# Kernel optimization log

Measured on AMD Instinct MI355X. Metric: run time of the kernel, lower is better.

Reference implementation:

```python
import jax, jax.numpy as jnp
import numpy as np

NUM_DEPTH_CANDIDATES = 32
CLAMP_MIN_DEPTH = 1e-3


def _vb(x):
    # rearrange 'b v ... -> (v b) ...'
    return jnp.reshape(jnp.swapaxes(x, 0, 1), (x.shape[0] * x.shape[1],) + x.shape[2:])


def _grid_sample_bilinear(img, u, v):
    # img: (N, C, H, W); u, v: (N, M) normalized to [-1, 1]; align_corners=True, zero padding
    N, C, H, W = img.shape
    ix = (u + 1.0) * 0.5 * (W - 1)
    iy = (v + 1.0) * 0.5 * (H - 1)
    x0 = jnp.floor(ix); y0 = jnp.floor(iy)
    x1 = x0 + 1.0; y1 = y0 + 1.0
    wx1 = ix - x0; wx0 = 1.0 - wx1
    wy1 = iy - y0; wy0 = 1.0 - wy1
    imgf = img.reshape(N, C, H * W)

    def gather(xi, yi):
        valid = (xi >= 0) & (xi <= W - 1) & (yi >= 0) & (yi <= H - 1)
        xc = jnp.clip(xi, 0, W - 1).astype(jnp.int32)
        yc = jnp.clip(yi, 0, H - 1).astype(jnp.int32)
        lin = yc * W + xc  # (N, M)
        vals = jax.vmap(lambda im, i: jnp.take(im, i, axis=1))(imgf, lin)  # (N, C, M)
        return vals * valid[:, None, :].astype(img.dtype)

    out = (gather(x0, y0) * (wx0 * wy0)[:, None, :]
           + gather(x1, y0) * (wx1 * wy0)[:, None, :]
           + gather(x0, y1) * (wx0 * wy1)[:, None, :]
           + gather(x1, y1) * (wx1 * wy1)[:, None, :])
    return out  # (N, C, M)


def _warp_with_pose_depth(feat1, pose, depth):
    # feat1: (N, C, H, W); pose: (N, 4, 4); depth: (N, D, H, W)
    N, C, H, W = feat1.shape
    D = depth.shape[1]
    two_pi = 2.0 * jnp.pi
    theta = (jnp.arange(W, dtype=jnp.float32) + 0.5) * (two_pi / W)  # longitude (W,)
    phi = (jnp.arange(H, dtype=jnp.float32) + 0.5) * (jnp.pi / H)    # colatitude (H,)
    sphi = jnp.sin(phi)[:, None]
    dirs = jnp.stack([sphi * jnp.sin(theta)[None, :],
                      jnp.broadcast_to(jnp.cos(phi)[:, None], (H, W)),
                      sphi * jnp.cos(theta)[None, :]], axis=-1)  # (H, W, 3) unit rays
    pts = depth[..., None] * dirs[None, None]                    # (N, D, H, W, 3)
    R = pose[:, :3, :3]
    t = pose[:, :3, 3]
    ptsw = jnp.einsum('nij,ndhwj->ndhwi', R, pts) + t[:, None, None, None, :]
    r = jnp.maximum(jnp.linalg.norm(ptsw, axis=-1), CLAMP_MIN_DEPTH)
    phi_w = jnp.arccos(jnp.clip(ptsw[..., 1] / r, -1.0, 1.0))
    theta_w = jnp.mod(jnp.arctan2(ptsw[..., 0], ptsw[..., 2]), two_pi)
    # spherical_2_equi then pixel->normalized [-1,1]
    u = theta_w / two_pi * 2.0 - 1.0
    v = phi_w / jnp.pi * 2.0 - 1.0
    M = D * H * W
    sampled = _grid_sample_bilinear(feat1, u.reshape(N, M), v.reshape(N, M))
    return sampled.reshape(N, C, D, H, W)


def _forward(features, extrinsics, near, far):
    b, v, c, h, w = features.shape  # v == 2
    feat0 = _vb(features)                       # (vb, c, h, w) reference features
    feat1 = _vb(features[:, ::-1])              # (vb, c, h, w) other-view features
    E0 = extrinsics[:, 0]
    E1 = extrinsics[:, 1]
    pose = jnp.linalg.inv(E1) @ E0              # ref->tgt (b,4,4)
    poses = jnp.concatenate([pose, jnp.linalg.inv(pose)], axis=0)  # (vb,4,4)
    # inverse-depth candidates, rearrange 'b v -> (v b) 1'
    mind = 1.0 / jnp.reshape(far.T, (-1, 1))
    maxd = 1.0 / jnp.reshape(near.T, (-1, 1))
    lin = jnp.linspace(0.0, 1.0, NUM_DEPTH_CANDIDATES, dtype=jnp.float32)
    depth_candi = 1.0 / (mind + lin[None, :] * (maxd - mind))  # (vb, D)
    depth = jnp.broadcast_to(depth_candi[:, :, None, None], (v * b, NUM_DEPTH_CANDIDATES, h, w))
    warped = _warp_with_pose_depth(feat1, poses, depth)        # (vb, c, D, h, w)
    corr = jnp.einsum('nchw,ncdhw->ndhw', feat0, warped) / (c ** 0.5)
    return corr  # (vb, D, h, w) plane-sweep cost volume


def setup_inputs() -> dict:
    key = jax.random.key(0)
    k1, k2, k3 = jax.random.split(key, 3)
    B, V, C, H, W = 1, 2, 128, 64, 128
    features = jax.random.normal(k1, (B, V, C, H, W), dtype=jnp.float32)
    # proper SE(3) extrinsics: random rotation via QR + small translation
    m = jax.random.normal(k2, (B, V, 3, 3), dtype=jnp.float32)
    q, _ = jnp.linalg.qr(m)
    q = q * jnp.linalg.det(q)[..., None, None]  # det +1
    t = jax.random.normal(k3, (B, V, 3), dtype=jnp.float32) * 0.1
    E = (jnp.zeros((B, V, 4, 4), dtype=jnp.float32)
         .at[..., :3, :3].set(q)
         .at[..., :3, 3].set(t)
         .at[..., 3, 3].set(1.0))
    near = jnp.full((B, V), 0.5, dtype=jnp.float32)
    far = jnp.full((B, V), 10.0, dtype=jnp.float32)
    return {"features": features, "extrinsics": E, "near": near, "far": far}


def reference(features, extrinsics, near, far):
    return _forward(features, extrinsics, near, far)
```

## Files before the change

### kernel.cpp

```cpp
#include <hip/hip_runtime.h>
#include <math.h>

#define V_ 2
#define C_ 128
#define H_ 64
#define W_ 128
#define D_ 32
#define HW_ (H_*W_)
#define PIXELS (V_*HW_)

#define PI_F 3.14159265358979323846f
#define TWO_PI_F 6.28318530717958647692f


__global__ __launch_bounds__(256) void transpose_kernel(const float* __restrict__ f,
                                                        float* __restrict__ T) {
  __shared__ float tile[64][W_ + 2];
  const int b = blockIdx.x;
  const int chalf = b & 1;
  const int h = (b >> 1) & (H_ - 1);
  const int v = b >> 7;
  const int c0 = chalf * 64;
  const int t = threadIdx.x;

  const float* src = f + (((size_t)(v * C_ + c0)) * H_ + h) * W_;
  {
    const int w2 = t & 63;
    const int cb = t >> 6;
#pragma unroll
    for (int p = 0; p < 16; ++p) {
      const int c = cb + p * 4;
      const float2 x = *(const float2*)(src + (size_t)c * HW_ + w2 * 2);
      tile[c][w2 * 2]     = x.x;
      tile[c][w2 * 2 + 1] = x.y;
    }
  }
  __syncthreads();
  float* dst = T + (((size_t)v * H_ + h) * W_) * C_ + c0;
  {
    const int c2 = t & 31;
    const int w0 = t >> 5;
#pragma unroll
    for (int p = 0; p < 16; ++p) {
      const int w = w0 + p * 8;
      float2 o;
      o.x = tile[2 * c2][w];
      o.y = tile[2 * c2 + 1][w];
      *(float2*)(dst + (size_t)w * C_ + 2 * c2) = o;
    }
  }
}

__device__ __forceinline__ float bperm_f(int byte_idx, float x) {
  return __int_as_float(__builtin_amdgcn_ds_bpermute(byte_idx, __float_as_int(x)));
}

__global__ __launch_bounds__(256, 4) void corr_kernel(const float* __restrict__ T,
                                                      const float* __restrict__ ex,
                                                      const float* __restrict__ nearp,
                                                      const float* __restrict__ farp,
                                                      float* __restrict__ out) {
  const int lane = threadIdx.x & 63;
  const int pix  = blockIdx.x * 4 + (threadIdx.x >> 6);
  const int n   = pix >> 13;
  const int rem = pix & 8191;
  const int h   = rem >> 7;
  const int w   = rem & 127;
  const int cg  = lane >> 5;
  const int cl  = lane & 31;

  const float* F0 = T + (size_t)n       * HW_ * C_;
  const float* F1 = T + (size_t)(1 - n) * HW_ * C_;

  const float4 f0v = *(const float4*)(F0 + ((size_t)(h * W_ + w)) * C_ + cl * 4);

  float PR[9], PT[3];
  {
    float R0[9], R1[9];
#pragma unroll
    for (int r = 0; r < 3; ++r)
#pragma unroll
      for (int c = 0; c < 3; ++c) {
        R0[r * 3 + c] = ex[r * 4 + c];
        R1[r * 3 + c] = ex[16 + r * 4 + c];
      }
    const float d0 = ex[3]  - ex[19];
    const float d1 = ex[7]  - ex[23];
    const float d2 = ex[11] - ex[27];
#pragma unroll
    for (int i = 0; i < 3; ++i) {
#pragma unroll
      for (int c = 0; c < 3; ++c)
        PR[i * 3 + c] = R1[i] * R0[c] + R1[3 + i] * R0[3 + c] + R1[6 + i] * R0[6 + c];
      PT[i] = R1[i] * d0 + R1[3 + i] * d1 + R1[6 + i] * d2;
    }
  }
  float Rm[9], tv[3];
  if (n == 0) {
#pragma unroll
    for (int i = 0; i < 9; ++i) Rm[i] = PR[i];
#pragma unroll
    for (int i = 0; i < 3; ++i) tv[i] = PT[i];
  } else {
#pragma unroll
    for (int r = 0; r < 3; ++r)
#pragma unroll
      for (int c = 0; c < 3; ++c) Rm[r * 3 + c] = PR[c * 3 + r];
#pragma unroll
    for (int r = 0; r < 3; ++r)
      tv[r] = -(PR[r] * PT[0] + PR[3 + r] * PT[1] + PR[6 + r] * PT[2]);
  }

  const float theta = ((float)w + 0.5f) * (TWO_PI_F / (float)W_);
  const float phi   = ((float)h + 0.5f) * (PI_F / (float)H_);
  const float sphi = sinf(phi);
  const float dx_ = sphi * sinf(theta);
  const float dy_ = cosf(phi);
  const float dz_ = sphi * cosf(theta);
  const float rdx = Rm[0] * dx_ + Rm[1] * dy_ + Rm[2] * dz_;
  const float rdy = Rm[3] * dx_ + Rm[4] * dy_ + Rm[5] * dz_;
  const float rdz = Rm[6] * dx_ + Rm[7] * dy_ + Rm[8] * dz_;

  const float mind = 1.f / farp[n];
  const float maxd = 1.f / nearp[n];
  const float depth = 1.f / (mind + ((float)cl / 31.f) * (maxd - mind));
  const float px = depth * rdx + tv[0];
  const float py = depth * rdy + tv[1];
  const float pz = depth * rdz + tv[2];
  float r = sqrtf(px * px + py * py + pz * pz);
  r = fmaxf(r, 0.001f);
  const float cy = fminf(fmaxf(py / r, -1.f), 1.f);
  const float phiw = acosf(cy);
  float thw = atan2f(px, pz);
  if (thw < 0.f) thw += TWO_PI_F;
  const float ix = thw * ((float)(W_ - 1) / TWO_PI_F);
  const float iy = phiw * ((float)(H_ - 1) / PI_F);

  const float x0f = floorf(ix), y0f = floorf(iy);
  const float x1f = x0f + 1.f,  y1f = y0f + 1.f;
  const float wx1 = ix - x0f, wx0 = 1.f - wx1;
  const float wy1 = iy - y0f, wy0 = 1.f - wy1;
  const float vx0 = (x0f >= 0.f && x0f <= (float)(W_ - 1)) ? 1.f : 0.f;
  const float vx1 = (x1f >= 0.f && x1f <= (float)(W_ - 1)) ? 1.f : 0.f;
  const float vy0 = (y0f >= 0.f && y0f <= (float)(H_ - 1)) ? 1.f : 0.f;
  const float vy1 = (y1f >= 0.f && y1f <= (float)(H_ - 1)) ? 1.f : 0.f;
  const int xi0 = (int)fminf(fmaxf(x0f, 0.f), (float)(W_ - 1));
  const int xi1 = (int)fminf(fmaxf(x1f, 0.f), (float)(W_ - 1));
  const int yi0 = (int)fminf(fmaxf(y0f, 0.f), (float)(H_ - 1));
  const int yi1 = (int)fminf(fmaxf(y1f, 0.f), (float)(H_ - 1));
  const float w00 = wx0 * wy0 * vx0 * vy0;
  const float w10 = wx1 * wy0 * vx1 * vy0;
  const float w01 = wx0 * wy1 * vx0 * vy1;
  const float w11 = wx1 * wy1 * vx1 * vy1;
  const float wA_pre = cg ? w10 : w00;
  const float wB_pre = cg ? w11 : w01;
  const int packed = ((yi0 * W_ + xi0) * C_) | ((xi1 - xi0) << 30) | ((yi1 - yi0) << 31);

  const int choff_b  = cl * 16;
  const int permbase = cg * 128;

  float acc[32];
#pragma unroll
  for (int d = 0; d < 32; ++d) {
    const int pk = __builtin_amdgcn_readlane(packed, d);
    const int bi    = pk & 0x000FFFFF;
    const int dxo_b = (int)(((unsigned)pk >> 21) & 512u);
    const int dyo_b = (int)(((unsigned)pk >> 31) << 16);
    const char* baseA = (const char*)(F1 + bi);
    const int vt   = choff_b + dxo_b;
    const int voff = cg ? vt : choff_b;
    const float4 sA = *(const float4*)(baseA + voff);
    const float4 sB = *(const float4*)(baseA + (dyo_b + voff));
    const float wa = bperm_f(permbase + d * 4, wA_pre);
    const float wb = bperm_f(permbase + d * 4, wB_pre);
    const float dota = sA.x * f0v.x + sA.y * f0v.y + sA.z * f0v.z + sA.w * f0v.w;
    const float dotb = sB.x * f0v.x + sB.y * f0v.y + sB.z * f0v.z + sB.w * f0v.w;
    acc[d] = wa * dota + wb * dotb;
  }

  float a16[16];
#pragma unroll
  for (int j = 0; j < 16; ++j) {
    const bool hi = (lane & 32) != 0;
    const float keep = hi ? acc[j + 16] : acc[j];
    const float send = hi ? acc[j] : acc[j + 16];
    a16[j] = keep + __shfl_xor(send, 32, 64);
  }
  float a8[8];
#pragma unroll
  for (int j = 0; j < 8; ++j) {
    const bool hi = (lane & 16) != 0;
    const float keep = hi ? a16[j + 8] : a16[j];
    const float send = hi ? a16[j] : a16[j + 8];
    a8[j] = keep + __shfl_xor(send, 16, 64);
  }
  float a4[4];
#pragma unroll
  for (int j = 0; j < 4; ++j) {
    const bool hi = (lane & 8) != 0;
    const float keep = hi ? a8[j + 4] : a8[j];
    const float send = hi ? a8[j] : a8[j + 4];
    a4[j] = keep + __shfl_xor(send, 8, 64);
  }
  float a2[2];
#pragma unroll
  for (int j = 0; j < 2; ++j) {
    const bool hi = (lane & 4) != 0;
    const float keep = hi ? a4[j + 2] : a4[j];
    const float send = hi ? a4[j] : a4[j + 2];
    a2[j] = keep + __shfl_xor(send, 4, 64);
  }
  float v1;
  {
    const bool hi = (lane & 2) != 0;
    const float keep = hi ? a2[1] : a2[0];
    const float send = hi ? a2[0] : a2[1];
    v1 = keep + __shfl_xor(send, 2, 64);
  }
  v1 += __shfl_xor(v1, 1, 64);

  if ((lane & 1) == 0) {
    const int d = (lane >> 1) & 31;
    out[(((size_t)n * D_ + d) * H_ + h) * W_ + w] = v1 * 0.08838834764831845f;
  }
}

extern "C" void kernel_launch(void* const* d_in, const int* in_sizes, int n_in,
                              void* d_out, int out_size, void* d_ws, size_t ws_size,
                              hipStream_t stream) {
  const float* features = (const float*)d_in[0];
  const float* extr     = (const float*)d_in[1];
  const float* nearp    = (const float*)d_in[2];
  const float* farp     = (const float*)d_in[3];
  float* out = (float*)d_out;
  float* T   = (float*)d_ws;

  hipLaunchKernelGGL(transpose_kernel, dim3(V_ * H_ * 2), dim3(256), 0, stream, features, T);
  hipLaunchKernelGGL(corr_kernel, dim3(PIXELS / 4), dim3(256), 0, stream,
                     T, extr, nearp, farp, out);
}
```

Baseline: 103.7 us.

## Store transposed features in fp16 and use packed dot2 with double-buffered gathers

The transpose kernel now writes the channel-last feature copy as fp16, which halves the gather traffic in the correlation kernel. The correlation kernel reorganises lanes so each lane loads 8 halves for one of the four bilinear corners and computes dot products with fdot2 instructions. It prefetches gathers in groups of 8 depths with double buffering, and applies the bilinear weights after a partial reduction with a permuted depth ordering. Reduced precision may change accuracy relative to the fp32 reference, and the larger buffers raise register pressure.

```diff
diff --git a/kernel.cpp b/kernel.cpp
--- a/kernel.cpp
+++ b/kernel.cpp
@@ -12,9 +12,20 @@
 #define PI_F 3.14159265358979323846f
 #define TWO_PI_F 6.28318530717958647692f
 
+typedef _Float16 half2_t __attribute__((ext_vector_type(2)));
+typedef _Float16 half8_t __attribute__((ext_vector_type(8)));
+
+
+__device__ __forceinline__ float fdot2f(half2_t a, half2_t b, float c) {
+#if __has_builtin(__builtin_amdgcn_fdot2)
+  return __builtin_amdgcn_fdot2(a, b, c, false);
+#else
+  return (float)a[0] * (float)b[0] + ((float)a[1] * (float)b[1] + c);
+#endif
+}
 
 __global__ __launch_bounds__(256) void transpose_kernel(const float* __restrict__ f,
-                                                        float* __restrict__ T) {
+                                                        _Float16* __restrict__ T) {
   __shared__ float tile[64][W_ + 2];
   const int b = blockIdx.x;
   const int chalf = b & 1;
@@ -36,17 +47,17 @@
     }
   }
   __syncthreads();
-  float* dst = T + (((size_t)v * H_ + h) * W_) * C_ + c0;
+  _Float16* dst = T + (((size_t)v * H_ + h) * W_) * C_ + c0;
   {
     const int c2 = t & 31;
     const int w0 = t >> 5;
 #pragma unroll
     for (int p = 0; p < 16; ++p) {
       const int w = w0 + p * 8;
-      float2 o;
-      o.x = tile[2 * c2][w];
-      o.y = tile[2 * c2 + 1][w];
-      *(float2*)(dst + (size_t)w * C_ + 2 * c2) = o;
+      half2_t o;
+      o[0] = (_Float16)tile[2 * c2][w];
+      o[1] = (_Float16)tile[2 * c2 + 1][w];
+      *(half2_t*)(dst + (size_t)w * C_ + 2 * c2) = o;
     }
   }
 }
@@ -55,7 +66,7 @@
   return __int_as_float(__builtin_amdgcn_ds_bpermute(byte_idx, __float_as_int(x)));
 }
 
-__global__ __launch_bounds__(256, 4) void corr_kernel(const float* __restrict__ T,
+__global__ __launch_bounds__(256, 4) void corr_kernel(const _Float16* __restrict__ T,
                                                       const float* __restrict__ ex,
                                                       const float* __restrict__ nearp,
                                                       const float* __restrict__ farp,
@@ -66,13 +77,18 @@
   const int rem = pix & 8191;
   const int h   = rem >> 7;
   const int w   = rem & 127;
-  const int cg  = lane >> 5;
-  const int cl  = lane & 31;
-
-  const float* F0 = T + (size_t)n       * HW_ * C_;
-  const float* F1 = T + (size_t)(1 - n) * HW_ * C_;
-
-  const float4 f0v = *(const float4*)(F0 + ((size_t)(h * W_ + w)) * C_ + cl * 4);
+  const int cl  = lane & 15;
+  const unsigned mx = ((lane >> 4) & 1) ? 0xFFFFFFFFu : 0u;
+  const unsigned my = (lane >= 32)     ? 0xFFFFFFFFu : 0u;
+
+  const char* F0b = (const char*)(T + (size_t)n       * HW_ * C_);
+  const char* F1b = (const char*)(T + (size_t)(1 - n) * HW_ * C_);
+
+  const half8_t f0v = *(const half8_t*)(F0b + ((size_t)(h * W_ + w)) * 256 + cl * 16);
+  const half2_t f0a = __builtin_shufflevector(f0v, f0v, 0, 1);
+  const half2_t f0b_ = __builtin_shufflevector(f0v, f0v, 2, 3);
+  const half2_t f0c = __builtin_shufflevector(f0v, f0v, 4, 5);
+  const half2_t f0d = __builtin_shufflevector(f0v, f0v, 6, 7);
 
   float PR[9], PT[3];
   {
@@ -121,9 +137,10 @@
   const float rdy = Rm[3] * dx_ + Rm[4] * dy_ + Rm[5] * dz_;
   const float rdz = Rm[6] * dx_ + Rm[7] * dy_ + Rm[8] * dz_;
 
+  const int dl = lane & 31;
   const float mind = 1.f / farp[n];
   const float maxd = 1.f / nearp[n];
-  const float depth = 1.f / (mind + ((float)cl / 31.f) * (maxd - mind));
+  const float depth = 1.f / (mind + ((float)dl / 31.f) * (maxd - mind));
   const float px = depth * rdx + tv[0];
   const float py = depth * rdy + tv[1];
   const float pz = depth * rdz + tv[2];
@@ -152,75 +169,106 @@
   const float w10 = wx1 * wy0 * vx1 * vy0;
   const float w01 = wx0 * wy1 * vx0 * vy1;
   const float w11 = wx1 * wy1 * vx1 * vy1;
-  const float wA_pre = cg ? w10 : w00;
-  const float wB_pre = cg ? w11 : w01;
-  const int packed = ((yi0 * W_ + xi0) * C_) | ((xi1 - xi0) << 30) | ((yi1 - yi0) << 31);
-
-  const int choff_b  = cl * 16;
-  const int permbase = cg * 128;
+  const float wA_pre = (lane >= 32) ? w10 : w00;
+  const float wB_pre = (lane >= 32) ? w11 : w01;
+  const unsigned packed = (unsigned)((yi0 * W_ + xi0) * 256)
+                        | ((unsigned)(xi1 - xi0) << 30)
+                        | ((unsigned)(yi1 - yi0) << 31);
+
+  const unsigned laneoff = (unsigned)(cl * 16);
+
+#define LOAD_DEPTH(d) ({                                                     \
+    const unsigned pk  = (unsigned)__builtin_amdgcn_readlane((int)packed, (d)); \
+    const unsigned sbi = pk & 0x3FFFFFu;                                     \
+    const unsigned sdx = (pk >> 22) & 256u;                                  \
+    const unsigned sdy = ((unsigned)((int)pk >> 31)) & 32768u;               \
+    const unsigned voff = sbi + (mx & sdx) + (my & sdy) + laneoff;           \
+    *(const half8_t*)(F1b + voff); })
 
   float acc[32];
-#pragma unroll
-  for (int d = 0; d < 32; ++d) {
-    const int pk = __builtin_amdgcn_readlane(packed, d);
-    const int bi    = pk & 0x000FFFFF;
-    const int dxo_b = (int)(((unsigned)pk >> 21) & 512u);
-    const int dyo_b = (int)(((unsigned)pk >> 31) << 16);
-    const char* baseA = (const char*)(F1 + bi);
-    const int vt   = choff_b + dxo_b;
-    const int voff = cg ? vt : choff_b;
-    const float4 sA = *(const float4*)(baseA + voff);
-    const float4 sB = *(const float4*)(baseA + (dyo_b + voff));
-    const float wa = bperm_f(permbase + d * 4, wA_pre);
-    const float wb = bperm_f(permbase + d * 4, wB_pre);
-    const float dota = sA.x * f0v.x + sA.y * f0v.y + sA.z * f0v.z + sA.w * f0v.w;
-    const float dotb = sB.x * f0v.x + sB.y * f0v.y + sB.z * f0v.z + sB.w * f0v.w;
-    acc[d] = wa * dota + wb * dotb;
-  }
+  half8_t buf0[8], buf1[8];
+#pragma unroll
+  for (int j = 0; j < 8; ++j) buf0[j] = LOAD_DEPTH(j);
+#pragma unroll
+  for (int dc = 0; dc < 4; ++dc) {
+    half8_t* cur = (dc & 1) ? buf1 : buf0;
+    half8_t* nxt = (dc & 1) ? buf0 : buf1;
+    if (dc < 3) {
+#pragma unroll
+      for (int j = 0; j < 8; ++j) nxt[j] = LOAD_DEPTH(dc * 8 + 8 + j);
+    }
+#pragma unroll
+    for (int j = 0; j < 8; ++j) {
+      const half8_t s = cur[j];
+      float dt = fdot2f(__builtin_shufflevector(s, s, 0, 1), f0a, 0.f);
+      dt = fdot2f(__builtin_shufflevector(s, s, 2, 3), f0b_, dt);
+      dt = fdot2f(__builtin_shufflevector(s, s, 4, 5), f0c, dt);
+      dt = fdot2f(__builtin_shufflevector(s, s, 6, 7), f0d, dt);
+      acc[dc * 8 + j] = dt;
+    }
+  }
+#undef LOAD_DEPTH
 
   float a16[16];
 #pragma unroll
   for (int j = 0; j < 16; ++j) {
-    const bool hi = (lane & 32) != 0;
+    const bool hi = (lane & 1) != 0;
     const float keep = hi ? acc[j + 16] : acc[j];
     const float send = hi ? acc[j] : acc[j + 16];
-    a16[j] = keep + __shfl_xor(send, 32, 64);
+    a16[j] = keep + __shfl_xor(send, 1, 64);
   }
   float a8[8];
 #pragma unroll
   for (int j = 0; j < 8; ++j) {
-    const bool hi = (lane & 16) != 0;
+    const bool hi = (lane & 2) != 0;
     const float keep = hi ? a16[j + 8] : a16[j];
     const float send = hi ? a16[j] : a16[j + 8];
-    a8[j] = keep + __shfl_xor(send, 16, 64);
+    a8[j] = keep + __shfl_xor(send, 2, 64);
   }
   float a4[4];
 #pragma unroll
   for (int j = 0; j < 4; ++j) {
-    const bool hi = (lane & 8) != 0;
+    const bool hi = (lane & 4) != 0;
     const float keep = hi ? a8[j + 4] : a8[j];
     const float send = hi ? a8[j] : a8[j + 4];
-    a4[j] = keep + __shfl_xor(send, 8, 64);
+    a4[j] = keep + __shfl_xor(send, 4, 64);
   }
   float a2[2];
 #pragma unroll
   for (int j = 0; j < 2; ++j) {
-    const bool hi = (lane & 4) != 0;
+    const bool hi = (lane & 8) != 0;
     const float keep = hi ? a4[j + 2] : a4[j];
     const float send = hi ? a4[j] : a4[j + 2];
-    a2[j] = keep + __shfl_xor(send, 4, 64);
-  }
+    a2[j] = keep + __shfl_xor(send, 8, 64);
+  }
+
+  {
+    const int dbase = ((lane & 1) << 4) | (((lane >> 1) & 1) << 3)
+                    | (((lane >> 2) & 1) << 2) | (((lane >> 3) & 1) << 1);
+    const int xsel = (lane >> 4) & 1;
+    const bool rowy1 = (lane & 32) != 0;
+#pragma unroll
+    for (int i = 0; i < 2; ++i) {
+      const int idx = (xsel * 32 + dbase + i) * 4;
+      const float wa = bperm_f(idx, wA_pre);
+      const float wb = bperm_f(idx, wB_pre);
+      a2[i] *= rowy1 ? wb : wa;
+    }
+  }
+
   float v1;
   {
-    const bool hi = (lane & 2) != 0;
+    const bool hi = (lane & 16) != 0;
     const float keep = hi ? a2[1] : a2[0];
     const float send = hi ? a2[0] : a2[1];
-    v1 = keep + __shfl_xor(send, 2, 64);
-  }
-  v1 += __shfl_xor(v1, 1, 64);
-
-  if ((lane & 1) == 0) {
-    const int d = (lane >> 1) & 31;
+    v1 = keep + __shfl_xor(send, 16, 64);
+  }
+  v1 += __shfl_xor(v1, 32, 64);
+
+  if (lane < 32) {
+    const int d = ((lane & 1) << 4) | (((lane >> 1) & 1) << 3)
+                | (((lane >> 2) & 1) << 2) | (((lane >> 3) & 1) << 1)
+                | ((lane >> 4) & 1);
     out[(((size_t)n * D_ + d) * H_ + h) * W_ + w] = v1 * 0.08838834764831845f;
   }
 }
@@ -233,7 +281,7 @@
   const float* nearp    = (const float*)d_in[2];
   const float* farp     = (const float*)d_in[3];
   float* out = (float*)d_out;
-  float* T   = (float*)d_ws;
+  _Float16* T = (_Float16*)d_ws;
 
   hipLaunchKernelGGL(transpose_kernel, dim3(V_ * H_ * 2), dim3(256), 0, stream, features, T);
   hipLaunchKernelGGL(corr_kernel, dim3(PIXELS / 4), dim3(256), 0, stream,
```

Result: faster. 91.11 us (-12.1%).
